# Kernel tuning notes

Measured on AMD Instinct MI355X. Metric: run time of the kernel, lower is better.

Reference implementation:

```python
import jax, jax.numpy as jnp
import numpy as np

D_MODEL = 32   # channels arg = Mamba d_model
D_INNER = 32   # expand=1
D_STATE = 8
DT_RANK = 2    # ceil(32/16)
D_CONV = 4


def layer_norm(h, g, b, eps=1e-5):
    m = jnp.mean(h, axis=-1, keepdims=True)
    v = jnp.var(h, axis=-1, keepdims=True)
    return (h - m) * jax.lax.rsqrt(v + eps) * g + b


def causal_conv1d(h, w, b):
    # h: [B, d, L]; w: [d, K] depthwise; torch Conv1d(padding=K-1) truncated to first L
    out = jax.lax.conv_general_dilated(h, w[:, None, :], (1,), [(D_CONV - 1, 0)],
                                       dimension_numbers=('NCH', 'OIH', 'NCH'),
                                       feature_group_count=h.shape[1])
    return out + b[None, :, None]


def selective_scan(u, delta, A, Bm, Cm, D):
    # u, delta: [B, d, L]; A: [d, n]; Bm, Cm: [B, n, L]; D: [d]
    dA = jnp.exp(jnp.einsum('bdl,dn->lbdn', delta, A))       # [L, B, d, n]
    dBu = jnp.einsum('bdl,bnl,bdl->lbdn', delta, Bm, u)      # [L, B, d, n]
    Cseq = jnp.transpose(Cm, (2, 0, 1))                      # [L, B, n]
    h0 = jnp.zeros((u.shape[0], A.shape[0], A.shape[1]), u.dtype)

    def step(h, inp):
        dA_t, dBu_t, C_t = inp
        h = dA_t * h + dBu_t
        return h, jnp.einsum('bdn,bn->bd', h, C_t)

    _, ys = jax.lax.scan(step, h0, (dA, dBu, Cseq))          # ys: [L, B, d]
    return jnp.transpose(ys, (1, 2, 0)) + D[None, :, None] * u


def mamba_direction(xz, conv_w, conv_b, xproj_w, dtproj_w, dtproj_b, A_log, D):
    xh, z = jnp.split(xz, 2, axis=1)                         # each [B, d_inner, L]
    xh = jax.nn.silu(causal_conv1d(xh, conv_w, conv_b))
    x_dbl = jnp.einsum('bdl,kd->bkl', xh, xproj_w)           # [B, dt_rank+2n, L]
    dt, Bm, Cm = jnp.split(x_dbl, [DT_RANK, DT_RANK + D_STATE], axis=1)
    dt = jax.nn.softplus(jnp.einsum('brl,dr->bdl', dt, dtproj_w) + dtproj_b[None, :, None])
    y = selective_scan(xh, dt, -jnp.exp(A_log), Bm, Cm, D)
    return y * jax.nn.silu(z)


def forward(x, lin1_w, lin1_b, ln1_g, ln1_b, in_proj_w,
            conv_w_f, conv_b_f, xproj_w_f, dtproj_w_f, dtproj_b_f, A_log_f, D_f,
            conv_w_r, conv_b_r, xproj_w_r, dtproj_w_r, dtproj_b_r, A_log_r, D_r,
            out_proj_w, mnorm_g, mnorm_b, lin2_w, lin2_b):
    avg = jnp.mean(x, axis=(2, 3))                           # [B, C] adaptive avg pool
    mx = jnp.max(x, axis=(2, 3))                             # [B, C] adaptive max pool
    combined = jnp.stack([avg, mx], axis=-1)                 # [B, C, 2]
    h = combined @ lin1_w.T + lin1_b                         # [B, C, d_model]
    h = layer_norm(h, ln1_g, ln1_b)
    # bidirectional Mamba (bimamba v2) over sequence length L = C
    xz = jnp.einsum('blc,ec->bel', h, in_proj_w)             # [B, 2*d_inner, L]
    out_f = mamba_direction(xz, conv_w_f, conv_b_f, xproj_w_f, dtproj_w_f, dtproj_b_f, A_log_f, D_f)
    out_r = mamba_direction(xz[..., ::-1], conv_w_r, conv_b_r, xproj_w_r, dtproj_w_r, dtproj_b_r, A_log_r, D_r)[..., ::-1]
    out = (out_f + out_r) / 2.0                              # if_devide_out=True
    out = jnp.einsum('bdl,od->blo', out, out_proj_w)         # [B, L, d_model]
    out = layer_norm(out, mnorm_g, mnorm_b)                  # use_norm=True
    att = jax.nn.sigmoid(out @ lin2_w.T + lin2_b)            # [B, L, 1]
    return att[..., None] * 0.25 + 0.875                     # [B, C, 1, 1]


def setup_inputs() -> dict:
    key = jax.random.key(0)
    ks = jax.random.split(key, 12)
    B, C, H, W = 32, 512, 64, 64

    def rn(k, shape, s):
        return jax.random.normal(k, shape, jnp.float32) * s

    A_log = jnp.log(jnp.broadcast_to(jnp.arange(1, D_STATE + 1, dtype=jnp.float32), (D_INNER, D_STATE)))
    return {
        'x': jax.random.normal(ks[0], (B, C, H, W), jnp.float32),
        'lin1_w': rn(ks[1], (D_MODEL, 2), 0.5),
        'lin1_b': jnp.zeros((D_MODEL,), jnp.float32),
        'ln1_g': jnp.ones((D_MODEL,), jnp.float32),
        'ln1_b': jnp.zeros((D_MODEL,), jnp.float32),
        'in_proj_w': rn(ks[2], (2 * D_INNER, D_MODEL), 0.1),
        'conv_w_f': rn(ks[3], (D_INNER, D_CONV), 0.3),
        'conv_b_f': jnp.zeros((D_INNER,), jnp.float32),
        'xproj_w_f': rn(ks[4], (DT_RANK + 2 * D_STATE, D_INNER), 0.1),
        'dtproj_w_f': rn(ks[5], (D_INNER, DT_RANK), 0.5),
        'dtproj_b_f': jnp.full((D_INNER,), -4.6, jnp.float32),
        'A_log_f': A_log,
        'D_f': jnp.ones((D_INNER,), jnp.float32),
        'conv_w_r': rn(ks[6], (D_INNER, D_CONV), 0.3),
        'conv_b_r': jnp.zeros((D_INNER,), jnp.float32),
        'xproj_w_r': rn(ks[7], (DT_RANK + 2 * D_STATE, D_INNER), 0.1),
        'dtproj_w_r': rn(ks[8], (D_INNER, DT_RANK), 0.5),
        'dtproj_b_r': jnp.full((D_INNER,), -4.6, jnp.float32),
        'A_log_r': A_log,
        'D_r': jnp.ones((D_INNER,), jnp.float32),
        'out_proj_w': rn(ks[9], (D_MODEL, D_INNER), 0.1),
        'mnorm_g': jnp.ones((D_MODEL,), jnp.float32),
        'mnorm_b': jnp.zeros((D_MODEL,), jnp.float32),
        'lin2_w': rn(ks[10], (1, D_MODEL), 0.3),
        'lin2_b': jnp.zeros((1,), jnp.float32),
    }


def reference(x, lin1_w, lin1_b, ln1_g, ln1_b, in_proj_w,
              conv_w_f, conv_b_f, xproj_w_f, dtproj_w_f, dtproj_b_f, A_log_f, D_f,
              conv_w_r, conv_b_r, xproj_w_r, dtproj_w_r, dtproj_b_r, A_log_r, D_r,
              out_proj_w, mnorm_g, mnorm_b, lin2_w, lin2_b):
    return forward(x, lin1_w, lin1_b, ln1_g, ln1_b, in_proj_w,
                   conv_w_f, conv_b_f, xproj_w_f, dtproj_w_f, dtproj_b_f, A_log_f, D_f,
                   conv_w_r, conv_b_r, xproj_w_r, dtproj_w_r, dtproj_b_r, A_log_r, D_r,
                   out_proj_w, mnorm_g, mnorm_b, lin2_w, lin2_b)
```

## Files before the change

### kernel.cpp

```cpp
#include <hip/hip_runtime.h>
#include <math.h>

#define BB 32
#define CC 512
#define HW 4096
#define DM 32
#define DI 32
#define DS 8
#define KC 4

#define NCH 16
#define CHL 32

__device__ __forceinline__ float siluf(float x) {
    return x / (1.0f + __expf(-x));
}
__device__ __forceinline__ float softplusf(float x) {
    float ax = fabsf(x);
    return fmaxf(x, 0.0f) + log1pf(__expf(-ax));
}

__global__ __launch_bounds__(256) void pool_kernel(const float* __restrict__ x,
                                                   float* __restrict__ avg,
                                                   float* __restrict__ mx) {
    int bc = blockIdx.x;
    const float4* xp = reinterpret_cast<const float4*>(x + (size_t)bc * HW);
    int tid = threadIdx.x;
    float s = 0.f, m = -INFINITY;
#pragma unroll
    for (int r = 0; r < 4; ++r) {
        float4 v = xp[r * 256 + tid];
        s += (v.x + v.y) + (v.z + v.w);
        m = fmaxf(m, fmaxf(fmaxf(v.x, v.y), fmaxf(v.z, v.w)));
    }
    for (int off = 32; off > 0; off >>= 1) {
        s += __shfl_down(s, off);
        m = fmaxf(m, __shfl_down(m, off));
    }
    __shared__ float ss[4], sm[4];
    int wave = tid >> 6;
    if ((tid & 63) == 0) { ss[wave] = s; sm[wave] = m; }
    __syncthreads();
    if (tid == 0) {
        float S = (ss[0] + ss[1]) + (ss[2] + ss[3]);
        float M = fmaxf(fmaxf(sm[0], sm[1]), fmaxf(sm[2], sm[3]));
        avg[bc] = S * (1.0f / HW);
        mx[bc]  = M;
    }
}

__global__ __launch_bounds__(256) void hproj_kernel(
    const float* __restrict__ avg, const float* __restrict__ mx,
    const float* __restrict__ lin1_w, const float* __restrict__ lin1_b,
    const float* __restrict__ ln1_g, const float* __restrict__ ln1_b,
    const float* __restrict__ in_proj_w, float* __restrict__ xz)
{
    __shared__ float sWp[64][33];
    int tid = threadIdx.x;
    for (int i = tid; i < 64 * DM; i += 256) sWp[i >> 5][i & 31] = in_proj_w[i];
    __syncthreads();

    int wave = tid >> 6, lane = tid & 63;
    int row = blockIdx.x * 4 + wave;
    float a = avg[row], M = mx[row];
    int m_ = lane & 31;
    float h = a * lin1_w[2 * m_] + M * lin1_w[2 * m_ + 1] + lin1_b[m_];
    float sum = h;
#pragma unroll
    for (int mask = 1; mask < 32; mask <<= 1) sum += __shfl_xor(sum, mask);
    float mean = sum * (1.0f / DM);
    float d = h - mean;
    float vs = d * d;
#pragma unroll
    for (int mask = 1; mask < 32; mask <<= 1) vs += __shfl_xor(vs, mask);
    float rs = rsqrtf(vs * (1.0f / DM) + 1e-5f);
    float hn = d * rs * ln1_g[m_] + ln1_b[m_];
    float acc = 0.f;
#pragma unroll
    for (int mm = 0; mm < DM; ++mm)
        acc += __shfl(hn, mm) * sWp[lane][mm];
    xz[((size_t)row << 6) + lane] = acc;
}

__global__ __launch_bounds__(256) void convscan1_kernel(
    const float* __restrict__ xz,
    const float* __restrict__ conv_w_f, const float* __restrict__ conv_b_f,
    const float* __restrict__ xproj_w_f, const float* __restrict__ dtproj_w_f,
    const float* __restrict__ dtproj_b_f,
    const float* __restrict__ conv_w_r, const float* __restrict__ conv_b_r,
    const float* __restrict__ xproj_w_r, const float* __restrict__ dtproj_w_r,
    const float* __restrict__ dtproj_b_r,
    const float* __restrict__ A_log_f, const float* __restrict__ A_log_r,
    float* __restrict__ u_g, float* __restrict__ dt_g,
    float* __restrict__ B_g, float* __restrict__ C_g,
    float* __restrict__ carrA, float* __restrict__ carrH)
{
    int bx = blockIdx.x;
    int bd = bx >> 4, j = bx & 15;
    int b = bd >> 1, dir = bd & 1;
    int tid = threadIdx.x;
    const float* cw = dir ? conv_w_r : conv_w_f;
    const float* cb = dir ? conv_b_r : conv_b_f;
    const float* xw = dir ? xproj_w_r : xproj_w_f;
    const float* dw = dir ? dtproj_w_r : dtproj_w_f;
    const float* db = dir ? dtproj_b_r : dtproj_b_f;
    const float* Alog = dir ? A_log_r : A_log_f;

    __shared__ float xt[32][39];
    __shared__ float xw_s[18][33];
    __shared__ float u_s[CHL][33];
    __shared__ float dt_s[CHL][33];
    __shared__ float B_s[CHL][9];
    __shared__ float C_s[CHL][9];
    __shared__ float dtr_s[CHL][2];

    for (int idx = tid; idx < 35 * 32; idx += 256) {
        int t = idx >> 5, dd = idx & 31;
        int sidx = j * CHL - 3 + t;
        float v = 0.f;
        if (sidx >= 0) {
            int orig = dir ? (511 - sidx) : sidx;
            v = xz[(((size_t)b * 512 + orig) << 6) + dd];
        }
        xt[dd][t] = v;
    }
    for (int idx = tid; idx < 18 * 32; idx += 256)
        xw_s[idx >> 5][idx & 31] = xw[idx];
    __syncthreads();

    int l = tid >> 3, g8 = tid & 7;
#pragma unroll
    for (int i = 0; i < 4; ++i) {
        int dd = g8 * 4 + i;
        float acc = cb[dd];
#pragma unroll
        for (int k = 0; k < KC; ++k) acc += cw[dd * KC + k] * xt[dd][l + k];
        u_s[l][dd] = siluf(acc);
    }
    __syncthreads();

    for (int o = g8; o < 18; o += 8) {
        float acc = 0.f;
#pragma unroll
        for (int m_ = 0; m_ < 32; ++m_) acc += u_s[l][m_] * xw_s[o][m_];
        if (o < 2) dtr_s[l][o] = acc;
        else if (o < 10) B_s[l][o - 2] = acc;
        else             C_s[l][o - 10] = acc;
    }
    __syncthreads();

    size_t rowbase = ((size_t)bd * 512 + j * CHL) * 32;
    for (int idx = tid; idx < CHL * 32; idx += 256) {
        int ll = idx >> 5, dd = idx & 31;
        float v = dtr_s[ll][0] * dw[dd * 2] + dtr_s[ll][1] * dw[dd * 2 + 1] + db[dd];
        float sp = softplusf(v);
        dt_s[ll][dd] = sp;
        dt_g[rowbase + idx] = sp;
        u_g[rowbase + idx] = u_s[ll][dd];
    }
    size_t base8 = ((size_t)bd * 512 + j * CHL) * 8;
    if (tid < CHL * 8) {
        B_g[base8 + tid] = B_s[tid >> 3][tid & 7];
        C_g[base8 + tid] = C_s[tid >> 3][tid & 7];
    }
    __syncthreads();

    int dd = tid >> 3, nn = tid & 7;
    float Aa = -__expf(Alog[tid]);
    float ap = 1.f, h = 0.f;
#pragma unroll 4
    for (int sl = 0; sl < CHL; ++sl) {
        float dtv = dt_s[sl][dd];
        float uu  = u_s[sl][dd];
        float bm  = B_s[sl][nn];
        float dA  = __expf(dtv * Aa);
        ap *= dA;
        h = dA * h + dtv * uu * bm;
    }
    carrA[((size_t)bx << 8) + tid] = ap;
    carrH[((size_t)bx << 8) + tid] = h;
}

__global__ __launch_bounds__(512) void scan2final_kernel(
    const float* __restrict__ u_g, const float* __restrict__ dt_g,
    const float* __restrict__ B_g, const float* __restrict__ C_g,
    const float* __restrict__ carrA, const float* __restrict__ carrH,
    const float* __restrict__ A_log_f, const float* __restrict__ D_f,
    const float* __restrict__ A_log_r, const float* __restrict__ D_r,
    const float* __restrict__ xz,
    const float* __restrict__ out_proj_w, const float* __restrict__ mnorm_g,
    const float* __restrict__ mnorm_b, const float* __restrict__ lin2_w,
    const float* __restrict__ lin2_b, float* __restrict__ out)
{
    int bx = blockIdx.x;
    int b = bx >> 4, t = bx & 15;
    int tid = threadIdx.x;
    int L0 = t * CHL;

    __shared__ float u_s[2][CHL][33];
    __shared__ float dt_s[2][CHL][33];
    __shared__ float B_s[2][CHL][12];
    __shared__ float C_s[2][CHL][12];
    __shared__ float z_s[CHL][33];
    __shared__ float y_s[2][CHL][33];
    __shared__ float comb_s[CHL][33];
    __shared__ float opw_s[DM][33];

    for (int idx = tid; idx < 2 * CHL * 32; idx += 512) {
        int dirw = idx >> 10;
        int r2 = idx & 1023;
        int sl = r2 >> 5, d = r2 & 31;
        int bd = b * 2 + dirw;
        int tc = dirw ? (15 - t) : t;
        size_t g = ((size_t)bd * 512 + tc * CHL + sl) * 32 + d;
        u_s[dirw][sl][d]  = u_g[g];
        dt_s[dirw][sl][d] = dt_g[g];
    }
    {
        int dirw = tid >> 8;
        int r2 = tid & 255;
        int sl = r2 >> 3, n = r2 & 7;
        int bd = b * 2 + dirw;
        int tc = dirw ? (15 - t) : t;
        size_t g = ((size_t)bd * 512 + tc * CHL + sl) * 8 + n;
        B_s[dirw][sl][n] = B_g[g];
        C_s[dirw][sl][n] = C_g[g];
    }
    for (int idx = tid; idx < CHL * 32; idx += 512) {
        int l = idx >> 5, d = idx & 31;
        z_s[l][d] = xz[(((size_t)b * 512 + L0 + l) << 6) + 32 + d];
        opw_s[idx >> 5][d] = out_proj_w[idx];
    }
    __syncthreads();

    {
        int dir = tid >> 8;
        int r = tid & 255;
        int d = r >> 3, n = r & 7;
        int bd = b * 2 + dir;
        int tt = dir ? (15 - t) : t;
        const float* Alog = dir ? A_log_r : A_log_f;
        const float* Dp   = dir ? D_r : D_f;
        float A  = -__expf(Alog[r]);
        float Dd = Dp[d];

        float h = 0.f;
        for (int g4 = 0; g4 < 4; ++g4) {
            int jbase = g4 * 4;
            if (jbase >= tt) break;
            float av[4], hv[4];
#pragma unroll
            for (int k = 0; k < 4; ++k) {
                int jj = jbase + k;
                int js = (jj < tt) ? jj : 0;
                size_t cb2 = (((size_t)bd * NCH + js) << 8) + r;
                av[k] = carrA[cb2];
                hv[k] = carrH[cb2];
            }
#pragma unroll
            for (int k = 0; k < 4; ++k)
                if (jbase + k < tt) h = av[k] * h + hv[k];
        }

#pragma unroll 4
        for (int sl = 0; sl < CHL; ++sl) {
            float dtv = dt_s[dir][sl][d];
            float uu  = u_s[dir][sl][d];
            float bm  = B_s[dir][sl][n];
            float cm  = C_s[dir][sl][n];
            h = __expf(dtv * A) * h + dtv * uu * bm;
            float py = h * cm;
            py += __shfl_xor(py, 1);
            py += __shfl_xor(py, 2);
            py += __shfl_xor(py, 4);
            if (n == 0) {
                int ll = dir ? (CHL - 1 - sl) : sl;
                y_s[dir][ll][d] = py + Dd * uu;
            }
        }
    }
    __syncthreads();

    for (int idx = tid; idx < CHL * 32; idx += 512) {
        int l = idx >> 5, d = idx & 31;
        comb_s[l][d] = 0.5f * (y_s[0][l][d] + y_s[1][l][d]) * siluf(z_s[l][d]);
    }
    __syncthreads();

    {
        int l = tid >> 4, k = tid & 15;
        float oa = 0.f, ob = 0.f;
#pragma unroll
        for (int d = 0; d < DI; ++d) {
            float c = comb_s[l][d];
            oa += c * opw_s[k][d];
            ob += c * opw_s[k + 16][d];
        }
        float sum = oa + ob;
#pragma unroll
        for (int mask = 1; mask < 16; mask <<= 1) sum += __shfl_xor(sum, mask);
        float mean = sum * (1.0f / DM);
        float da = oa - mean, db2 = ob - mean;
        float vs = da * da + db2 * db2;
#pragma unroll
        for (int mask = 1; mask < 16; mask <<= 1) vs += __shfl_xor(vs, mask);
        float rs = rsqrtf(vs * (1.0f / DM) + 1e-5f);
        float va = da * rs * mnorm_g[k] + mnorm_b[k];
        float vb = db2 * rs * mnorm_g[k + 16] + mnorm_b[k + 16];
        float sv = va * lin2_w[k] + vb * lin2_w[k + 16];
#pragma unroll
        for (int mask = 1; mask < 16; mask <<= 1) sv += __shfl_xor(sv, mask);
        if (k == 0) {
            float att = 1.0f / (1.0f + __expf(-(sv + lin2_b[0])));
            out[(size_t)b * 512 + L0 + l] = 0.25f * att + 0.875f;
        }
    }
}

extern "C" void kernel_launch(void* const* d_in, const int* in_sizes, int n_in,
                              void* d_out, int out_size, void* d_ws, size_t ws_size,
                              hipStream_t stream)
{
    const float* x         = (const float*)d_in[0];
    const float* lin1_w    = (const float*)d_in[1];
    const float* lin1_b    = (const float*)d_in[2];
    const float* ln1_g     = (const float*)d_in[3];
    const float* ln1_b     = (const float*)d_in[4];
    const float* in_proj_w = (const float*)d_in[5];
    const float* conv_w_f  = (const float*)d_in[6];
    const float* conv_b_f  = (const float*)d_in[7];
    const float* xproj_w_f = (const float*)d_in[8];
    const float* dtproj_w_f= (const float*)d_in[9];
    const float* dtproj_b_f= (const float*)d_in[10];
    const float* A_log_f   = (const float*)d_in[11];
    const float* D_f       = (const float*)d_in[12];
    const float* conv_w_r  = (const float*)d_in[13];
    const float* conv_b_r  = (const float*)d_in[14];
    const float* xproj_w_r = (const float*)d_in[15];
    const float* dtproj_w_r= (const float*)d_in[16];
    const float* dtproj_b_r= (const float*)d_in[17];
    const float* A_log_r   = (const float*)d_in[18];
    const float* D_r       = (const float*)d_in[19];
    const float* out_proj_w= (const float*)d_in[20];
    const float* mnorm_g   = (const float*)d_in[21];
    const float* mnorm_b   = (const float*)d_in[22];
    const float* lin2_w    = (const float*)d_in[23];
    const float* lin2_b    = (const float*)d_in[24];

    float* ws   = (float*)d_ws;
    float* avg  = ws;
    float* mx   = ws + 16384;
    float* xz   = ws + 32768;
    float* u_g  = xz + 1048576;
    float* dt_g = u_g + 1048576;
    float* B_g  = dt_g + 1048576;
    float* C_g  = B_g + 262144;
    float* carrA= C_g + 262144;
    float* carrH= carrA + 262144;
    (void)ws_size; (void)in_sizes; (void)n_in; (void)out_size;

    pool_kernel<<<BB * CC, 256, 0, stream>>>(x, avg, mx);
    hproj_kernel<<<4096, 256, 0, stream>>>(avg, mx, lin1_w, lin1_b, ln1_g, ln1_b, in_proj_w, xz);
    convscan1_kernel<<<BB * 2 * NCH, 256, 0, stream>>>(
        xz, conv_w_f, conv_b_f, xproj_w_f, dtproj_w_f, dtproj_b_f,
        conv_w_r, conv_b_r, xproj_w_r, dtproj_w_r, dtproj_b_r,
        A_log_f, A_log_r, u_g, dt_g, B_g, C_g, carrA, carrH);
    scan2final_kernel<<<BB * NCH, 512, 0, stream>>>(
        u_g, dt_g, B_g, C_g, carrA, carrH,
        A_log_f, D_f, A_log_r, D_r, xz,
        out_proj_w, mnorm_g, mnorm_b, lin2_w, lin2_b, (float*)d_out);
}
```

Before: 86.76 us.

## Fuse input projection into scan kernels and recompute intermediates instead of storing

Removes the separate hproj kernel and the global xz, u, dt, B and C buffers. Both scan kernels now recompute the layer norm, in_proj, conv, x_proj and dt_proj on chip from the pooled avg/max values. This cuts a kernel launch and several MB of global traffic, but duplicates the projection and conv work in the second kernel and uses more shared memory per block, which may lower occupancy.

```diff
diff --git a/kernel.cpp b/kernel.cpp
--- a/kernel.cpp
+++ b/kernel.cpp
@@ -49,41 +49,11 @@
     }
 }
 
-__global__ __launch_bounds__(256) void hproj_kernel(
+__global__ __launch_bounds__(256) void convscan1_kernel(
     const float* __restrict__ avg, const float* __restrict__ mx,
     const float* __restrict__ lin1_w, const float* __restrict__ lin1_b,
     const float* __restrict__ ln1_g, const float* __restrict__ ln1_b,
-    const float* __restrict__ in_proj_w, float* __restrict__ xz)
-{
-    __shared__ float sWp[64][33];
-    int tid = threadIdx.x;
-    for (int i = tid; i < 64 * DM; i += 256) sWp[i >> 5][i & 31] = in_proj_w[i];
-    __syncthreads();
-
-    int wave = tid >> 6, lane = tid & 63;
-    int row = blockIdx.x * 4 + wave;
-    float a = avg[row], M = mx[row];
-    int m_ = lane & 31;
-    float h = a * lin1_w[2 * m_] + M * lin1_w[2 * m_ + 1] + lin1_b[m_];
-    float sum = h;
-#pragma unroll
-    for (int mask = 1; mask < 32; mask <<= 1) sum += __shfl_xor(sum, mask);
-    float mean = sum * (1.0f / DM);
-    float d = h - mean;
-    float vs = d * d;
-#pragma unroll
-    for (int mask = 1; mask < 32; mask <<= 1) vs += __shfl_xor(vs, mask);
-    float rs = rsqrtf(vs * (1.0f / DM) + 1e-5f);
-    float hn = d * rs * ln1_g[m_] + ln1_b[m_];
-    float acc = 0.f;
-#pragma unroll
-    for (int mm = 0; mm < DM; ++mm)
-        acc += __shfl(hn, mm) * sWp[lane][mm];
-    xz[((size_t)row << 6) + lane] = acc;
-}
-
-__global__ __launch_bounds__(256) void convscan1_kernel(
-    const float* __restrict__ xz,
+    const float* __restrict__ in_proj_w,
     const float* __restrict__ conv_w_f, const float* __restrict__ conv_b_f,
     const float* __restrict__ xproj_w_f, const float* __restrict__ dtproj_w_f,
     const float* __restrict__ dtproj_b_f,
@@ -91,8 +61,6 @@
     const float* __restrict__ xproj_w_r, const float* __restrict__ dtproj_w_r,
     const float* __restrict__ dtproj_b_r,
     const float* __restrict__ A_log_f, const float* __restrict__ A_log_r,
-    float* __restrict__ u_g, float* __restrict__ dt_g,
-    float* __restrict__ B_g, float* __restrict__ C_g,
     float* __restrict__ carrA, float* __restrict__ carrH)
 {
     int bx = blockIdx.x;
@@ -106,26 +74,58 @@
     const float* db = dir ? dtproj_b_r : dtproj_b_f;
     const float* Alog = dir ? A_log_r : A_log_f;
 
+    __shared__ float h_s[35][33];
     __shared__ float xt[32][39];
-    __shared__ float xw_s[18][33];
+    __shared__ float sWx[32][33];
+    __shared__ float xw_s[10][33];
     __shared__ float u_s[CHL][33];
     __shared__ float dt_s[CHL][33];
     __shared__ float B_s[CHL][9];
-    __shared__ float C_s[CHL][9];
     __shared__ float dtr_s[CHL][2];
 
-    for (int idx = tid; idx < 35 * 32; idx += 256) {
-        int t = idx >> 5, dd = idx & 31;
-        int sidx = j * CHL - 3 + t;
-        float v = 0.f;
-        if (sidx >= 0) {
+    for (int idx = tid; idx < 32 * 32; idx += 256) sWx[idx >> 5][idx & 31] = in_proj_w[idx];
+    for (int idx = tid; idx < 10 * 32; idx += 256) xw_s[idx >> 5][idx & 31] = xw[idx];
+
+#pragma unroll
+    for (int p = 0; p < 5; ++p) {
+        int idx = p * 256 + tid;
+        int c = idx >> 5, m = idx & 31;
+        float hn = 0.f;
+        if (c < 35) {
+            int sidx = j * CHL - 3 + c;
             int orig = dir ? (511 - sidx) : sidx;
-            v = xz[(((size_t)b * 512 + orig) << 6) + dd];
-        }
-        xt[dd][t] = v;
-    }
-    for (int idx = tid; idx < 18 * 32; idx += 256)
-        xw_s[idx >> 5][idx & 31] = xw[idx];
+            float a = 0.f, M = 0.f;
+            if (sidx >= 0) { a = avg[(b << 9) + orig]; M = mx[(b << 9) + orig]; }
+            float h = a * lin1_w[2 * m] + M * lin1_w[2 * m + 1] + lin1_b[m];
+            float sum = h;
+#pragma unroll
+            for (int mask = 1; mask < 32; mask <<= 1) sum += __shfl_xor(sum, mask);
+            float mean = sum * (1.0f / DM);
+            float d = h - mean;
+            float vs = d * d;
+#pragma unroll
+            for (int mask = 1; mask < 32; mask <<= 1) vs += __shfl_xor(vs, mask);
+            float rs = rsqrtf(vs * (1.0f / DM) + 1e-5f);
+            hn = d * rs * ln1_g[m] + ln1_b[m];
+            h_s[c][m] = hn;
+        }
+    }
+    __syncthreads();
+
+#pragma unroll
+    for (int p = 0; p < 5; ++p) {
+        int idx = p * 256 + tid;
+        int c = idx >> 5, d = idx & 31;
+        if (c < 35) {
+            int sidx = j * CHL - 3 + c;
+            float acc = 0.f;
+            if (sidx >= 0) {
+#pragma unroll
+                for (int mm = 0; mm < DM; ++mm) acc += h_s[c][mm] * sWx[d][mm];
+            }
+            xt[d][c] = acc;
+        }
+    }
     __syncthreads();
 
     int l = tid >> 3, g8 = tid & 7;
@@ -139,29 +139,19 @@
     }
     __syncthreads();
 
-    for (int o = g8; o < 18; o += 8) {
+    for (int o = g8; o < 10; o += 8) {
         float acc = 0.f;
 #pragma unroll
         for (int m_ = 0; m_ < 32; ++m_) acc += u_s[l][m_] * xw_s[o][m_];
         if (o < 2) dtr_s[l][o] = acc;
-        else if (o < 10) B_s[l][o - 2] = acc;
-        else             C_s[l][o - 10] = acc;
-    }
-    __syncthreads();
-
-    size_t rowbase = ((size_t)bd * 512 + j * CHL) * 32;
+        else       B_s[l][o - 2] = acc;
+    }
+    __syncthreads();
+
     for (int idx = tid; idx < CHL * 32; idx += 256) {
         int ll = idx >> 5, dd = idx & 31;
         float v = dtr_s[ll][0] * dw[dd * 2] + dtr_s[ll][1] * dw[dd * 2 + 1] + db[dd];
-        float sp = softplusf(v);
-        dt_s[ll][dd] = sp;
-        dt_g[rowbase + idx] = sp;
-        u_g[rowbase + idx] = u_s[ll][dd];
-    }
-    size_t base8 = ((size_t)bd * 512 + j * CHL) * 8;
-    if (tid < CHL * 8) {
-        B_g[base8 + tid] = B_s[tid >> 3][tid & 7];
-        C_g[base8 + tid] = C_s[tid >> 3][tid & 7];
+        dt_s[ll][dd] = softplusf(v);
     }
     __syncthreads();
 
@@ -182,12 +172,19 @@
 }
 
 __global__ __launch_bounds__(512) void scan2final_kernel(
-    const float* __restrict__ u_g, const float* __restrict__ dt_g,
-    const float* __restrict__ B_g, const float* __restrict__ C_g,
+    const float* __restrict__ avg, const float* __restrict__ mx,
+    const float* __restrict__ lin1_w, const float* __restrict__ lin1_b,
+    const float* __restrict__ ln1_g, const float* __restrict__ ln1_b,
+    const float* __restrict__ in_proj_w,
     const float* __restrict__ carrA, const float* __restrict__ carrH,
+    const float* __restrict__ conv_w_f, const float* __restrict__ conv_b_f,
+    const float* __restrict__ xproj_w_f, const float* __restrict__ dtproj_w_f,
+    const float* __restrict__ dtproj_b_f,
+    const float* __restrict__ conv_w_r, const float* __restrict__ conv_b_r,
+    const float* __restrict__ xproj_w_r, const float* __restrict__ dtproj_w_r,
+    const float* __restrict__ dtproj_b_r,
     const float* __restrict__ A_log_f, const float* __restrict__ D_f,
     const float* __restrict__ A_log_r, const float* __restrict__ D_r,
-    const float* __restrict__ xz,
     const float* __restrict__ out_proj_w, const float* __restrict__ mnorm_g,
     const float* __restrict__ mnorm_b, const float* __restrict__ lin2_w,
     const float* __restrict__ lin2_b, float* __restrict__ out)
@@ -197,39 +194,118 @@
     int tid = threadIdx.x;
     int L0 = t * CHL;
 
+    __shared__ float h_s[38][33];
+    __shared__ float xt[32][41];
+    __shared__ float z_s[CHL][33];
+    __shared__ float sW[64][33];
+    __shared__ float xw_s[2][18][33];
     __shared__ float u_s[2][CHL][33];
     __shared__ float dt_s[2][CHL][33];
-    __shared__ float B_s[2][CHL][12];
-    __shared__ float C_s[2][CHL][12];
-    __shared__ float z_s[CHL][33];
+    __shared__ float B_s[2][CHL][9];
+    __shared__ float C_s[2][CHL][9];
+    __shared__ float dtr_s[2][CHL][2];
     __shared__ float y_s[2][CHL][33];
     __shared__ float comb_s[CHL][33];
     __shared__ float opw_s[DM][33];
 
-    for (int idx = tid; idx < 2 * CHL * 32; idx += 512) {
-        int dirw = idx >> 10;
-        int r2 = idx & 1023;
-        int sl = r2 >> 5, d = r2 & 31;
-        int bd = b * 2 + dirw;
-        int tc = dirw ? (15 - t) : t;
-        size_t g = ((size_t)bd * 512 + tc * CHL + sl) * 32 + d;
-        u_s[dirw][sl][d]  = u_g[g];
-        dt_s[dirw][sl][d] = dt_g[g];
-    }
-    {
-        int dirw = tid >> 8;
-        int r2 = tid & 255;
-        int sl = r2 >> 3, n = r2 & 7;
-        int bd = b * 2 + dirw;
-        int tc = dirw ? (15 - t) : t;
-        size_t g = ((size_t)bd * 512 + tc * CHL + sl) * 8 + n;
-        B_s[dirw][sl][n] = B_g[g];
-        C_s[dirw][sl][n] = C_g[g];
+    for (int idx = tid; idx < 64 * 32; idx += 512) sW[idx >> 5][idx & 31] = in_proj_w[idx];
+    for (int idx = tid; idx < 2 * 18 * 32; idx += 512) {
+        int dirw = idx >= 576;
+        int r2 = idx - dirw * 576;
+        const float* xw = dirw ? xproj_w_r : xproj_w_f;
+        xw_s[dirw][r2 >> 5][r2 & 31] = xw[r2];
+    }
+    for (int idx = tid; idx < DM * 32; idx += 512) opw_s[idx >> 5][idx & 31] = out_proj_w[idx];
+
+#pragma unroll
+    for (int p = 0; p < 3; ++p) {
+        int idx = p * 512 + tid;
+        int c = idx >> 5, m = idx & 31;
+        if (c < 38) {
+            int col = L0 - 3 + c;
+            float a = 0.f, M = 0.f;
+            if (col >= 0 && col < 512) { a = avg[(b << 9) + col]; M = mx[(b << 9) + col]; }
+            float h = a * lin1_w[2 * m] + M * lin1_w[2 * m + 1] + lin1_b[m];
+            float sum = h;
+#pragma unroll
+            for (int mask = 1; mask < 32; mask <<= 1) sum += __shfl_xor(sum, mask);
+            float mean = sum * (1.0f / DM);
+            float d = h - mean;
+            float vs = d * d;
+#pragma unroll
+            for (int mask = 1; mask < 32; mask <<= 1) vs += __shfl_xor(vs, mask);
+            float rs = rsqrtf(vs * (1.0f / DM) + 1e-5f);
+            h_s[c][m] = d * rs * ln1_g[m] + ln1_b[m];
+        }
+    }
+    __syncthreads();
+
+#pragma unroll
+    for (int p = 0; p < 3; ++p) {
+        int idx = p * 512 + tid;
+        int c = idx >> 5, d = idx & 31;
+        if (c < 38) {
+            int col = L0 - 3 + c;
+            float acc = 0.f;
+            if (col >= 0 && col < 512) {
+#pragma unroll
+                for (int mm = 0; mm < DM; ++mm) acc += h_s[c][mm] * sW[d][mm];
+            }
+            xt[d][c] = acc;
+        }
     }
     for (int idx = tid; idx < CHL * 32; idx += 512) {
         int l = idx >> 5, d = idx & 31;
-        z_s[l][d] = xz[(((size_t)b * 512 + L0 + l) << 6) + 32 + d];
-        opw_s[idx >> 5][d] = out_proj_w[idx];
+        float acc = 0.f;
+#pragma unroll
+        for (int mm = 0; mm < DM; ++mm) acc += h_s[l + 3][mm] * sW[32 + d][mm];
+        z_s[l][d] = acc;
+    }
+    __syncthreads();
+
+#pragma unroll
+    for (int p = 0; p < 4; ++p) {
+        int idx = p * 512 + tid;
+        int dd = idx & 31, l = (idx >> 5) & 31, dirw = idx >> 10;
+        const float* cw2 = dirw ? conv_w_r : conv_w_f;
+        const float* cb2 = dirw ? conv_b_r : conv_b_f;
+        float acc = cb2[dd];
+        if (dirw == 0) {
+#pragma unroll
+            for (int k = 0; k < KC; ++k) acc += cw2[dd * KC + k] * xt[dd][l + k];
+        } else {
+#pragma unroll
+            for (int jj = 0; jj < KC; ++jj) acc += cw2[dd * KC + 3 - jj] * xt[dd][l + 3 + jj];
+        }
+        u_s[dirw][l][dd] = siluf(acc);
+    }
+    __syncthreads();
+
+#pragma unroll
+    for (int p = 0; p < 3; ++p) {
+        int idx = p * 512 + tid;
+        if (idx < 1152) {
+            int dirw = idx >= 576;
+            int r2 = idx - dirw * 576;
+            int o = r2 >> 5, l = r2 & 31;
+            float acc = 0.f;
+#pragma unroll
+            for (int m_ = 0; m_ < 32; ++m_) acc += u_s[dirw][l][m_] * xw_s[dirw][o][m_];
+            if (o < 2)       dtr_s[dirw][l][o] = acc;
+            else if (o < 10) B_s[dirw][l][o - 2] = acc;
+            else             C_s[dirw][l][o - 10] = acc;
+        }
+    }
+    __syncthreads();
+
+#pragma unroll
+    for (int p = 0; p < 4; ++p) {
+        int idx = p * 512 + tid;
+        int dd = idx & 31, l = (idx >> 5) & 31, dirw = idx >> 10;
+        const float* dw2 = dirw ? dtproj_w_r : dtproj_w_f;
+        const float* db2 = dirw ? dtproj_b_r : dtproj_b_f;
+        float v = dtr_s[dirw][l][0] * dw2[dd * 2] + dtr_s[dirw][l][1] * dw2[dd * 2 + 1] + db2[dd];
+        dt_s[dirw][l][dd] = softplusf(v);
     }
     __syncthreads();
 
@@ -264,19 +340,17 @@
 
 #pragma unroll 4
         for (int sl = 0; sl < CHL; ++sl) {
-            float dtv = dt_s[dir][sl][d];
-            float uu  = u_s[dir][sl][d];
-            float bm  = B_s[dir][sl][n];
-            float cm  = C_s[dir][sl][n];
+            int ll = dir ? (CHL - 1 - sl) : sl;
+            float dtv = dt_s[dir][ll][d];
+            float uu  = u_s[dir][ll][d];
+            float bm  = B_s[dir][ll][n];
+            float cm  = C_s[dir][ll][n];
             h = __expf(dtv * A) * h + dtv * uu * bm;
             float py = h * cm;
             py += __shfl_xor(py, 1);
             py += __shfl_xor(py, 2);
             py += __shfl_xor(py, 4);
-            if (n == 0) {
-                int ll = dir ? (CHL - 1 - sl) : sl;
-                y_s[dir][ll][d] = py + Dd * uu;
-            }
+            if (n == 0) y_s[dir][ll][d] = py + Dd * uu;
         }
     }
     __syncthreads();
@@ -350,23 +424,21 @@
     float* ws   = (float*)d_ws;
     float* avg  = ws;
     float* mx   = ws + 16384;
-    float* xz   = ws + 32768;
-    float* u_g  = xz + 1048576;
-    float* dt_g = u_g + 1048576;
-    float* B_g  = dt_g + 1048576;
-    float* C_g  = B_g + 262144;
-    float* carrA= C_g + 262144;
+    float* carrA= ws + 32768;
     float* carrH= carrA + 262144;
     (void)ws_size; (void)in_sizes; (void)n_in; (void)out_size;
 
     pool_kernel<<<BB * CC, 256, 0, stream>>>(x, avg, mx);
-    hproj_kernel<<<4096, 256, 0, stream>>>(avg, mx, lin1_w, lin1_b, ln1_g, ln1_b, in_proj_w, xz);
     convscan1_kernel<<<BB * 2 * NCH, 256, 0, stream>>>(
-        xz, conv_w_f, conv_b_f, xproj_w_f, dtproj_w_f, dtproj_b_f,
+        avg, mx, lin1_w, lin1_b, ln1_g, ln1_b, in_proj_w,
+        conv_w_f, conv_b_f, xproj_w_f, dtproj_w_f, dtproj_b_f,
         conv_w_r, conv_b_r, xproj_w_r, dtproj_w_r, dtproj_b_r,
-        A_log_f, A_log_r, u_g, dt_g, B_g, C_g, carrA, carrH);
+        A_log_f, A_log_r, carrA, carrH);
     scan2final_kernel<<<BB * NCH, 512, 0, stream>>>(
-        u_g, dt_g, B_g, C_g, carrA, carrH,
-        A_log_f, D_f, A_log_r, D_r, xz,
+        avg, mx, lin1_w, lin1_b, ln1_g, ln1_b, in_proj_w,
+        carrA, carrH,
+        conv_w_f, conv_b_f, xproj_w_f, dtproj_w_f, dtproj_b_f,
+        conv_w_r, conv_b_r, xproj_w_r, dtproj_w_r, dtproj_b_r,
+        A_log_f, D_f, A_log_r, D_r,
         out_proj_w, mnorm_g, mnorm_b, lin2_w, lin2_b, (float*)d_out);
 }
```

New measurement: 89.96 us. +3.7%, slower.
